# Kernel optimization log

Measured on AMD Instinct MI355X. Metric: run time of the kernel, lower is better.

Reference implementation:

```python
import jax, jax.numpy as jnp
import numpy as np

D_MODEL = 1024
N_HEAD = 16
N_KV_HEAD = 4
HEAD_DIM = D_MODEL // N_HEAD  # 64
N_GROUP = N_HEAD // N_KV_HEAD  # 4
ROPE_BASE = 10000.0
ROPE_DIM = HEAD_DIM  # rope_percentage = 1.0


def _rope_tables(seq_len, dtype):
    half = ROPE_DIM // 2
    inv_freq = 1.0 / (ROPE_BASE ** (jnp.arange(0, half, dtype=jnp.float32) * 2.0 / ROPE_DIM))
    pos = jnp.arange(seq_len, dtype=jnp.float32)
    freqs = pos[:, None] * inv_freq[None, :]  # [S, half]
    return jnp.cos(freqs).astype(dtype), jnp.sin(freqs).astype(dtype)


def _apply_rope(t):
    # t: [B, H, S, D]; rotate first ROPE_DIM dims (split-half convention)
    S = t.shape[2]
    cos, sin = _rope_tables(S, t.dtype)  # [S, half]
    half = ROPE_DIM // 2
    t1 = t[..., :half]
    t2 = t[..., half:ROPE_DIM]
    rot = jnp.concatenate([t1 * cos - t2 * sin, t1 * sin + t2 * cos], axis=-1)
    if ROPE_DIM < t.shape[-1]:
        rot = jnp.concatenate([rot, t[..., ROPE_DIM:]], axis=-1)
    return rot


def setup_inputs() -> dict:
    key = jax.random.key(0)
    ks = jax.random.split(key, 5)
    B, S = 1, 4096
    sd = 1.0 / np.sqrt(D_MODEL)
    x = jax.random.normal(ks[0], (B, S, D_MODEL), dtype=jnp.float32)
    w_q = jax.random.normal(ks[1], (D_MODEL, N_HEAD * HEAD_DIM), dtype=jnp.float32) * sd
    w_k = jax.random.normal(ks[2], (D_MODEL, N_KV_HEAD * HEAD_DIM), dtype=jnp.float32) * sd
    w_v = jax.random.normal(ks[3], (D_MODEL, N_KV_HEAD * HEAD_DIM), dtype=jnp.float32) * sd
    w_o = jax.random.normal(ks[4], (D_MODEL, D_MODEL), dtype=jnp.float32) * sd
    return {"x": x, "w_q": w_q, "w_k": w_k, "w_v": w_v, "w_o": w_o}


def reference(x, w_q, w_k, w_v, w_o):
    B, S, _ = x.shape
    q = (x @ w_q).reshape(B, S, N_HEAD, HEAD_DIM).transpose(0, 2, 1, 3)     # [B,H,S,D]
    k = (x @ w_k).reshape(B, S, N_KV_HEAD, HEAD_DIM).transpose(0, 2, 1, 3)  # [B,Hk,S,D]
    v = (x @ w_v).reshape(B, S, N_KV_HEAD, HEAD_DIM).transpose(0, 2, 1, 3)
    q = _apply_rope(q)
    k = _apply_rope(k)
    # repeat KV heads to match query heads (ops.repeat along head axis)
    k = jnp.repeat(k, N_GROUP, axis=1)  # [B,H,S,D]
    v = jnp.repeat(v, N_GROUP, axis=1)
    scale = 1.0 / jnp.sqrt(jnp.asarray(HEAD_DIM, dtype=x.dtype))
    scores = jnp.einsum("bhqd,bhkd->bhqk", q, k) * scale
    attn = jax.nn.softmax(scores, axis=-1)
    out = jnp.einsum("bhqk,bhkd->bhqd", attn, v)  # [B,H,S,D]
    out = out.transpose(0, 2, 1, 3).reshape(B, S, D_MODEL)
    return out @ w_o
```

## Files before the change

### kernel.cpp

```cpp
#include <hip/hip_runtime.h>
#include <math.h>

#define S_LEN 4096
#define DMODEL 1024
#define NHEAD 16
#define NKV 4
#define HDIM 64
#define QSCALE 0.125f

typedef __attribute__((ext_vector_type(8))) short bf16x8;
typedef __attribute__((ext_vector_type(4))) float f32x4;

static __device__ __forceinline__ unsigned short f2bf(float f) {
  unsigned int u = __float_as_uint(f);
  u += 0x7fffu + ((u >> 16) & 1u);
  return (unsigned short)(u >> 16);
}

static __device__ __forceinline__ void gload_lds16(const unsigned short* g, unsigned short* l) {
  __builtin_amdgcn_global_load_lds((const __attribute__((address_space(1))) void*)g,
                                   (__attribute__((address_space(3))) void*)l, 16, 0, 0);
}

__global__ void k_cast4(const float* __restrict__ in, unsigned short* __restrict__ out) {
  int i = blockIdx.x * blockDim.x + threadIdx.x;
  if (i >= S_LEN * DMODEL / 4) return;
  f32x4 v = *(const f32x4*)(in + (size_t)i * 4);
  union { unsigned short us[4]; uint2 d; } o;
#pragma unroll
  for (int j = 0; j < 4; ++j) o.us[j] = f2bf(v[j]);
  *(uint2*)(out + (size_t)i * 4) = o.d;
}

__global__ __launch_bounds__(256) void k_prepw(const float* __restrict__ wq, const float* __restrict__ wk,
                                               const float* __restrict__ wv, const float* __restrict__ wo,
                                               unsigned short* __restrict__ wqkvT, unsigned short* __restrict__ woT) {
  __shared__ float T[64][65];
  int b = blockIdx.x;
  const float* src;
  unsigned short* dst;
  int srcN, n0, k0, scol;
  if (b < 384) {
    int rt = b >> 4, kt = b & 15;
    n0 = rt * 64; k0 = kt * 64;
    if (n0 < 1024) { src = wq; srcN = 1024; scol = n0; }
    else if (n0 < 1280) { src = wk; srcN = 256; scol = n0 - 1024; }
    else { src = wv; srcN = 256; scol = n0 - 1280; }
    dst = wqkvT;
  } else {
    int bb = b - 384;
    int rt = bb >> 4, kt = bb & 15;
    n0 = rt * 64; k0 = kt * 64;
    src = wo; srcN = 1024; scol = n0; dst = woT;
  }
  int tr = threadIdx.x >> 6, tc = threadIdx.x & 63;
#pragma unroll
  for (int i = 0; i < 16; ++i) {
    int kk = i * 4 + tr;
    T[kk][tc] = src[(size_t)(k0 + kk) * srcN + scol + tc];
  }
  __syncthreads();
#pragma unroll
  for (int i = 0; i < 16; ++i) {
    int nn = i * 4 + tr;
    dst[(size_t)(n0 + nn) * 1024 + k0 + tc] = f2bf(T[tc][nn]);
  }
}

__global__ void k_rope_tables(float* __restrict__ ct, float* __restrict__ st) {
  int i = blockIdx.x * blockDim.x + threadIdx.x;
  if (i >= S_LEN * 32) return;
  int s = i >> 5, d = i & 31;
  float inv = expf(-(float)d * (1.0f / 32.0f) * logf(10000.0f));
  float f = (float)s * inv;
  ct[i] = cosf(f);
  st[i] = sinf(f);
}

__global__ __launch_bounds__(256) void k_gemmQKV(const unsigned short* __restrict__ A,
                                                 const unsigned short* __restrict__ BT,
                                                 const float* __restrict__ ct, const float* __restrict__ st,
                                                 unsigned short* __restrict__ Qb, unsigned short* __restrict__ Kh,
                                                 unsigned short* __restrict__ Vb) {
  __shared__ unsigned short As[128 * 64];
  __shared__ unsigned short Bs[128 * 64];
  const int tid = threadIdx.x;
  const int lane = tid & 63, wid = tid >> 6;
  const int r = lane & 15, g = lane >> 4;
  const int wm = wid >> 1, wn = wid & 1;
  const int bn0 = blockIdx.x << 7;
  const int bm0 = blockIdx.y << 7;

  f32x4 acc[4][4];
#pragma unroll
  for (int mt = 0; mt < 4; ++mt)
#pragma unroll
    for (int nt = 0; nt < 4; ++nt) acc[mt][nt] = 0.0f;

  for (int k0 = 0; k0 < 1024; k0 += 64) {
#pragma unroll
    for (int i = 0; i < 4; ++i) {
      int c = i * 256 + tid;
      int row = c >> 3, slot = c & 7;
      int ss = slot ^ (row & 7);
      int lbase = (i * 256 + (tid & ~63)) * 8;
      gload_lds16(A + (size_t)(bm0 + row) * 1024 + k0 + ss * 8, &As[lbase]);
      gload_lds16(BT + (size_t)(bn0 + row) * 1024 + k0 + ss * 8, &Bs[lbase]);
    }
    __syncthreads();
#pragma unroll
    for (int h = 0; h < 2; ++h) {
      bf16x8 am[4], bn[4];
#pragma unroll
      for (int mt = 0; mt < 4; ++mt) {
        int row = wm * 64 + mt * 16 + r;
        int slot = (g + 4 * h) ^ (row & 7);
        am[mt] = *(const bf16x8*)&As[row * 64 + slot * 8];
      }
#pragma unroll
      for (int nt = 0; nt < 4; ++nt) {
        int row = wn * 64 + nt * 16 + r;
        int slot = (g + 4 * h) ^ (row & 7);
        bn[nt] = *(const bf16x8*)&Bs[row * 64 + slot * 8];
      }
#pragma unroll
      for (int mt = 0; mt < 4; ++mt)
#pragma unroll
        for (int nt = 0; nt < 4; ++nt)
          acc[mt][nt] = __builtin_amdgcn_mfma_f32_16x16x32_bf16(am[mt], bn[nt], acc[mt][nt], 0, 0, 0);
    }
    __syncthreads();
  }

  const int colbase = bn0 + wn * 64;
  const int srow0 = bm0 + wm * 64;
  if (colbase < 1024) {
#pragma unroll
    for (int mt = 0; mt < 4; ++mt)
#pragma unroll
      for (int q = 0; q < 4; ++q) {
        int srow = srow0 + mt * 16 + g * 4 + q;
#pragma unroll
        for (int ntp = 0; ntp < 2; ++ntp) {
          int di = ntp * 16 + r;
          float t1 = acc[mt][ntp][q], t2 = acc[mt][ntp + 2][q];
          float c = ct[srow * 32 + di], s = st[srow * 32 + di];
          Qb[(size_t)srow * 1024 + colbase + di] = f2bf((t1 * c - t2 * s) * QSCALE);
          Qb[(size_t)srow * 1024 + colbase + di + 32] = f2bf((t1 * s + t2 * c) * QSCALE);
        }
      }
  } else if (colbase < 1280) {
    const int kvh = (colbase - 1024) >> 6;
#pragma unroll
    for (int mt = 0; mt < 4; ++mt)
#pragma unroll
      for (int q = 0; q < 4; ++q) {
        int srow = srow0 + mt * 16 + g * 4 + q;
#pragma unroll
        for (int ntp = 0; ntp < 2; ++ntp) {
          int di = ntp * 16 + r;
          float t1 = acc[mt][ntp][q], t2 = acc[mt][ntp + 2][q];
          float c = ct[srow * 32 + di], s = st[srow * 32 + di];
          Kh[((size_t)kvh * S_LEN + srow) * 64 + di] = f2bf(t1 * c - t2 * s);
          Kh[((size_t)kvh * S_LEN + srow) * 64 + di + 32] = f2bf(t1 * s + t2 * c);
        }
      }
  } else {
    const int vcol = colbase - 1280;
#pragma unroll
    for (int mt = 0; mt < 4; ++mt)
#pragma unroll
      for (int nt = 0; nt < 4; ++nt)
#pragma unroll
        for (int q = 0; q < 4; ++q)
          Vb[(size_t)(srow0 + mt * 16 + g * 4 + q) * 256 + vcol + nt * 16 + r] = f2bf(acc[mt][nt][q]);
  }
}

__global__ void k_vperm(const unsigned short* __restrict__ Vb, unsigned short* __restrict__ VP) {
  int i4 = blockIdx.x * blockDim.x + threadIdx.x;
  if (i4 >= NKV * HDIM * S_LEN / 4) return;
  int i = i4 * 4;
  int s = i & (S_LEN - 1);
  int d = (i >> 12) & 63;
  int kvh = i >> 18;
  int base = s & ~63;
  int p64 = s & 63;
  int u = p64 >> 5, g = (p64 >> 3) & 3, jq = (p64 >> 2) & 1;
  int koff0 = 32 * u + 16 * jq + 4 * g;
  const unsigned short* src = Vb + (size_t)(base + koff0) * 256 + kvh * 64 + d;
  union { unsigned short us[4]; uint2 dd; } o;
#pragma unroll
  for (int j = 0; j < 4; ++j) o.us[j] = src[(size_t)j * 256];
  *(uint2*)(VP + i) = o.dd;
}

__global__ __launch_bounds__(256) void k_gemm128(const unsigned short* __restrict__ A,
                                                 const unsigned short* __restrict__ BT,
                                                 float* __restrict__ C, int M, int N, int K) {
  __shared__ unsigned short As[128 * 64];
  __shared__ unsigned short Bs[128 * 64];
  const int tid = threadIdx.x;
  const int lane = tid & 63, wid = tid >> 6;
  const int r = lane & 15, g = lane >> 4;
  const int wm = wid >> 1, wn = wid & 1;
  const int bn0 = blockIdx.x << 7;
  const int bm0 = blockIdx.y << 7;

  f32x4 acc[4][4];
#pragma unroll
  for (int mt = 0; mt < 4; ++mt)
#pragma unroll
    for (int nt = 0; nt < 4; ++nt) acc[mt][nt] = 0.0f;

  for (int k0 = 0; k0 < K; k0 += 64) {
#pragma unroll
    for (int i = 0; i < 4; ++i) {
      int c = i * 256 + tid;
      int row = c >> 3, slot = c & 7;
      int ss = slot ^ (row & 7);
      int lbase = (i * 256 + (tid & ~63)) * 8;
      gload_lds16(A + (size_t)(bm0 + row) * K + k0 + ss * 8, &As[lbase]);
      gload_lds16(BT + (size_t)(bn0 + row) * K + k0 + ss * 8, &Bs[lbase]);
    }
    __syncthreads();
#pragma unroll
    for (int h = 0; h < 2; ++h) {
      bf16x8 am[4], bn[4];
#pragma unroll
      for (int mt = 0; mt < 4; ++mt) {
        int row = wm * 64 + mt * 16 + r;
        int slot = (g + 4 * h) ^ (row & 7);
        am[mt] = *(const bf16x8*)&As[row * 64 + slot * 8];
      }
#pragma unroll
      for (int nt = 0; nt < 4; ++nt) {
        int row = wn * 64 + nt * 16 + r;
        int slot = (g + 4 * h) ^ (row & 7);
        bn[nt] = *(const bf16x8*)&Bs[row * 64 + slot * 8];
      }
#pragma unroll
      for (int mt = 0; mt < 4; ++mt)
#pragma unroll
        for (int nt = 0; nt < 4; ++nt)
          acc[mt][nt] = __builtin_amdgcn_mfma_f32_16x16x32_bf16(am[mt], bn[nt], acc[mt][nt], 0, 0, 0);
    }
    __syncthreads();
  }
#pragma unroll
  for (int mt = 0; mt < 4; ++mt)
#pragma unroll
    for (int nt = 0; nt < 4; ++nt)
#pragma unroll
      for (int q = 0; q < 4; ++q)
        C[(size_t)(bm0 + wm * 64 + mt * 16 + g * 4 + q) * N + bn0 + wn * 64 + nt * 16 + r] = acc[mt][nt][q];
}

__global__ __launch_bounds__(256, 2) void k_attn(const unsigned short* __restrict__ Q,
                                                 const unsigned short* __restrict__ Kh,
                                                 const unsigned short* __restrict__ VP,
                                                 unsigned short* __restrict__ Ab) {
  __shared__ unsigned short sm[2][2][4096];
  const int tid = threadIdx.x;
  const int wave = tid >> 6, lane = tid & 63;
  const int r = lane & 15, g = lane >> 4;
  const int kvh = blockIdx.y;
  const int head = kvh * 4 + wave;
  const int qbase = blockIdx.x * 32;
  const int bidx = (lane & 48) >> 2;

  const unsigned short* khb = Kh + (size_t)kvh * S_LEN * 64;
  const unsigned short* vpb = VP + (size_t)kvh * S_LEN * 64;

  bf16x8 qf[2][2];
#pragma unroll
  for (int c = 0; c < 2; ++c)
#pragma unroll
    for (int h0 = 0; h0 < 2; ++h0)
      qf[c][h0] = *(const bf16x8*)(Q + (size_t)(qbase + 16 * c + r) * DMODEL + head * HDIM + 32 * h0 + 8 * g);

  f32x4 Oa[2][4];
#pragma unroll
  for (int c = 0; c < 2; ++c)
#pragma unroll
    for (int dt = 0; dt < 4; ++dt) Oa[c][dt] = 0.0f;
  float m_[2] = {-INFINITY, -INFINITY};
  float l_[2] = {0.0f, 0.0f};

  auto stage = [&](int b, int kv0) {
#pragma unroll
    for (int i = 0; i < 2; ++i) {
      int row = i * 32 + (tid >> 3), slot = tid & 7;
      int cs = slot ^ (row & 7);
      int lbase = (i * 256 + (tid & ~63)) * 8;
      gload_lds16(khb + (size_t)(kv0 + row) * 64 + cs * 8, &sm[b][0][lbase]);
      gload_lds16(vpb + (size_t)row * S_LEN + kv0 + cs * 8, &sm[b][1][lbase]);
    }
  };

  stage(0, 0);
  asm volatile("s_waitcnt vmcnt(0)" ::: "memory");
  __syncthreads();

  for (int t = 0; t < 64; ++t) {
    const int buf = t & 1;
    if (t < 63) stage(buf ^ 1, (t + 1) * 64);

    bf16x8 kf[4][2], vf[4][2];
#pragma unroll
    for (int tt = 0; tt < 4; ++tt) {
      int row = 16 * tt + r;
#pragma unroll
      for (int h = 0; h < 2; ++h) {
        int slot = (g + 4 * h) ^ (r & 7);
        kf[tt][h] = *(const bf16x8*)&sm[buf][0][row * 64 + slot * 8];
        vf[tt][h] = *(const bf16x8*)&sm[buf][1][row * 64 + slot * 8];
      }
    }
    f32x4 sc[2][4];
#pragma unroll
    for (int tt = 0; tt < 4; ++tt)
#pragma unroll
      for (int c = 0; c < 2; ++c) {
        f32x4 a = 0.0f;
        a = __builtin_amdgcn_mfma_f32_16x16x32_bf16(kf[tt][0], qf[c][0], a, 0, 0, 0);
        a = __builtin_amdgcn_mfma_f32_16x16x32_bf16(kf[tt][1], qf[c][1], a, 0, 0, 0);
        sc[c][tt] = a;
      }
    bf16x8 pa[2][2];
    bool resc[2];
    float bsc[2][4];
#pragma unroll
    for (int c = 0; c < 2; ++c) {
      float a0 = fmaxf(fmaxf(sc[c][0][0], sc[c][0][1]), fmaxf(sc[c][0][2], sc[c][0][3]));
      float a1 = fmaxf(fmaxf(sc[c][1][0], sc[c][1][1]), fmaxf(sc[c][1][2], sc[c][1][3]));
      float a2 = fmaxf(fmaxf(sc[c][2][0], sc[c][2][1]), fmaxf(sc[c][2][2], sc[c][2][3]));
      float a3 = fmaxf(fmaxf(sc[c][3][0], sc[c][3][1]), fmaxf(sc[c][3][2], sc[c][3][3]));
      float tm = fmaxf(fmaxf(a0, a1), fmaxf(a2, a3));
      tm = fmaxf(tm, __shfl_xor(tm, 16, 64));
      tm = fmaxf(tm, __shfl_xor(tm, 32, 64));
      bool defer = __all(tm <= m_[c] + 8.0f);
      float mn = m_[c];
      float scl = 1.0f;
      if (!defer) {
        mn = fmaxf(m_[c], tm);
        scl = __expf(m_[c] - mn);
        m_[c] = mn;
      }
      resc[c] = !defer;
      float s0 = 0.f, s1 = 0.f, s2 = 0.f, s3 = 0.f;
#pragma unroll
      for (int p = 0; p < 4; ++p) {
        sc[c][0][p] = __expf(sc[c][0][p] - mn); s0 += sc[c][0][p];
        sc[c][1][p] = __expf(sc[c][1][p] - mn); s1 += sc[c][1][p];
        sc[c][2][p] = __expf(sc[c][2][p] - mn); s2 += sc[c][2][p];
        sc[c][3][p] = __expf(sc[c][3][p] - mn); s3 += sc[c][3][p];
      }
      float ts = (s0 + s1) + (s2 + s3);
      ts += __shfl_xor(ts, 16, 64);
      ts += __shfl_xor(ts, 32, 64);
      l_[c] = l_[c] * scl + ts;
      if (!defer) {
#pragma unroll
        for (int p = 0; p < 4; ++p) bsc[c][p] = __shfl(scl, bidx + p, 64);
      }
#pragma unroll
      for (int u = 0; u < 2; ++u) {
        union { bf16x8 v; unsigned short us[8]; } pk;
#pragma unroll
        for (int j = 0; j < 4; ++j) {
          pk.us[j] = f2bf(sc[c][2 * u][j]);
          pk.us[4 + j] = f2bf(sc[c][2 * u + 1][j]);
        }
        pa[c][u] = pk.v;
      }
    }
#pragma unroll
    for (int c = 0; c < 2; ++c)
      if (resc[c]) {
#pragma unroll
        for (int dt = 0; dt < 4; ++dt)
#pragma unroll
          for (int p = 0; p < 4; ++p) Oa[c][dt][p] *= bsc[c][p];
      }
#pragma unroll
    for (int dt = 0; dt < 4; ++dt)
#pragma unroll
      for (int c = 0; c < 2; ++c) {
        Oa[c][dt] = __builtin_amdgcn_mfma_f32_16x16x32_bf16(pa[c][0], vf[dt][0], Oa[c][dt], 0, 0, 0);
        Oa[c][dt] = __builtin_amdgcn_mfma_f32_16x16x32_bf16(pa[c][1], vf[dt][1], Oa[c][dt], 0, 0, 0);
      }
    asm volatile("s_waitcnt vmcnt(0)" ::: "memory");
    __syncthreads();
  }
#pragma unroll
  for (int c = 0; c < 2; ++c) {
    float li = 1.0f / l_[c];
    float bl[4];
#pragma unroll
    for (int p = 0; p < 4; ++p) bl[p] = __shfl(li, bidx + p, 64);
#pragma unroll
    for (int dt = 0; dt < 4; ++dt)
#pragma unroll
      for (int p = 0; p < 4; ++p)
        Ab[(size_t)(qbase + 16 * c + 4 * g + p) * DMODEL + head * HDIM + 16 * dt + r] =
            f2bf(Oa[c][dt][p] * bl[p]);
  }
}

extern "C" void kernel_launch(void* const* d_in, const int* in_sizes, int n_in,
                              void* d_out, int out_size, void* d_ws, size_t ws_size,
                              hipStream_t stream) {
  const float* x   = (const float*)d_in[0];
  const float* w_q = (const float*)d_in[1];
  const float* w_k = (const float*)d_in[2];
  const float* w_v = (const float*)d_in[3];
  const float* w_o = (const float*)d_in[4];
  float* out = (float*)d_out;

  char* ws = (char*)d_ws;
  size_t off = 0;
  auto alloc = [&](size_t bytes) -> void* {
    void* p = ws + off;
    off = (off + bytes + 255) & ~(size_t)255;
    return p;
  };
  unsigned short* xb    = (unsigned short*)alloc((size_t)S_LEN * DMODEL * 2);
  unsigned short* wqkvT = (unsigned short*)alloc((size_t)1536 * DMODEL * 2);
  unsigned short* woT   = (unsigned short*)alloc((size_t)DMODEL * DMODEL * 2);
  float* ct = (float*)alloc((size_t)S_LEN * 32 * 4);
  float* st = (float*)alloc((size_t)S_LEN * 32 * 4);
  unsigned short* Qb = (unsigned short*)alloc((size_t)S_LEN * DMODEL * 2);
  unsigned short* Kh = (unsigned short*)alloc((size_t)NKV * S_LEN * HDIM * 2);
  unsigned short* Vb = (unsigned short*)alloc((size_t)S_LEN * 256 * 2);
  unsigned short* VP = (unsigned short*)alloc((size_t)NKV * HDIM * S_LEN * 2);
  unsigned short* Ab = (unsigned short*)alloc((size_t)S_LEN * DMODEL * 2);

  k_cast4<<<(S_LEN * DMODEL / 4 + 255) / 256, 256, 0, stream>>>(x, xb);
  k_prepw<<<640, 256, 0, stream>>>(w_q, w_k, w_v, w_o, wqkvT, woT);
  k_rope_tables<<<(S_LEN * 32 + 255) / 256, 256, 0, stream>>>(ct, st);

  k_gemmQKV<<<dim3(1536 / 128, S_LEN / 128), 256, 0, stream>>>(xb, wqkvT, ct, st, Qb, Kh, Vb);
  k_vperm<<<(NKV * HDIM * S_LEN / 4 + 255) / 256, 256, 0, stream>>>(Vb, VP);

  k_attn<<<dim3(S_LEN / 32, NKV), 256, 0, stream>>>(Qb, Kh, VP, Ab);

  k_gemm128<<<dim3(DMODEL / 128, S_LEN / 128), 256, 0, stream>>>(Ab, woT, out, S_LEN, DMODEL, DMODEL);
}
```

Before: 256.4 us.

## Halve attention query tile per block and use exp2 with deferred row reductions

```diff
diff --git a/kernel.cpp b/kernel.cpp
--- a/kernel.cpp
+++ b/kernel.cpp
@@ -1,4 +1,5 @@
 #include <hip/hip_runtime.h>
+#include <hip/hip_bf16.h>
 #include <math.h>
 
 #define S_LEN 4096
@@ -6,7 +7,7 @@
 #define NHEAD 16
 #define NKV 4
 #define HDIM 64
-#define QSCALE 0.125f
+#define QSCALE 0.18033688011112042f
 
 typedef __attribute__((ext_vector_type(8))) short bf16x8;
 typedef __attribute__((ext_vector_type(4))) float f32x4;
@@ -15,6 +16,16 @@
   unsigned int u = __float_as_uint(f);
   u += 0x7fffu + ((u >> 16) & 1u);
   return (unsigned short)(u >> 16);
+}
+
+static __device__ __forceinline__ unsigned short f2bf_hw(float f) {
+  union { __hip_bfloat16 h; unsigned short u; } cv;
+  cv.h = __float2bfloat16(f);
+  return cv.u;
+}
+
+static __device__ __forceinline__ float fexp2(float x) {
+  return __builtin_amdgcn_exp2f(x);
 }
 
 static __device__ __forceinline__ void gload_lds16(const unsigned short* g, unsigned short* l) {
@@ -256,7 +267,7 @@
         C[(size_t)(bm0 + wm * 64 + mt * 16 + g * 4 + q) * N + bn0 + wn * 64 + nt * 16 + r] = acc[mt][nt][q];
 }
 
-__global__ __launch_bounds__(256, 2) void k_attn(const unsigned short* __restrict__ Q,
+__global__ __launch_bounds__(256, 4) void k_attn(const unsigned short* __restrict__ Q,
                                                  const unsigned short* __restrict__ Kh,
                                                  const unsigned short* __restrict__ VP,
                                                  unsigned short* __restrict__ Ab) {
@@ -264,28 +275,25 @@
   const int tid = threadIdx.x;
   const int wave = tid >> 6, lane = tid & 63;
   const int r = lane & 15, g = lane >> 4;
-  const int kvh = blockIdx.y;
+  const int bid = blockIdx.x;
+  const int kvh = bid & 3;
+  const int qbase = (((bid >> 3) << 1) + ((bid >> 2) & 1)) * 16;
   const int head = kvh * 4 + wave;
-  const int qbase = blockIdx.x * 32;
   const int bidx = (lane & 48) >> 2;
 
   const unsigned short* khb = Kh + (size_t)kvh * S_LEN * 64;
   const unsigned short* vpb = VP + (size_t)kvh * S_LEN * 64;
 
-  bf16x8 qf[2][2];
-#pragma unroll
-  for (int c = 0; c < 2; ++c)
-#pragma unroll
-    for (int h0 = 0; h0 < 2; ++h0)
-      qf[c][h0] = *(const bf16x8*)(Q + (size_t)(qbase + 16 * c + r) * DMODEL + head * HDIM + 32 * h0 + 8 * g);
-
-  f32x4 Oa[2][4];
-#pragma unroll
-  for (int c = 0; c < 2; ++c)
-#pragma unroll
-    for (int dt = 0; dt < 4; ++dt) Oa[c][dt] = 0.0f;
-  float m_[2] = {-INFINITY, -INFINITY};
-  float l_[2] = {0.0f, 0.0f};
+  bf16x8 qf[2];
+#pragma unroll
+  for (int h0 = 0; h0 < 2; ++h0)
+    qf[h0] = *(const bf16x8*)(Q + (size_t)(qbase + r) * DMODEL + head * HDIM + 32 * h0 + 8 * g);
+
+  f32x4 Oa[4];
+#pragma unroll
+  for (int dt = 0; dt < 4; ++dt) Oa[dt] = 0.0f;
+  float m_ = -INFINITY;
+  float l_ = 0.0f;
 
   auto stage = [&](int b, int kv0) {
 #pragma unroll
@@ -317,95 +325,79 @@
         vf[tt][h] = *(const bf16x8*)&sm[buf][1][row * 64 + slot * 8];
       }
     }
-    f32x4 sc[2][4];
-#pragma unroll
-    for (int tt = 0; tt < 4; ++tt)
-#pragma unroll
-      for (int c = 0; c < 2; ++c) {
-        f32x4 a = 0.0f;
-        a = __builtin_amdgcn_mfma_f32_16x16x32_bf16(kf[tt][0], qf[c][0], a, 0, 0, 0);
-        a = __builtin_amdgcn_mfma_f32_16x16x32_bf16(kf[tt][1], qf[c][1], a, 0, 0, 0);
-        sc[c][tt] = a;
-      }
-    bf16x8 pa[2][2];
-    bool resc[2];
-    float bsc[2][4];
-#pragma unroll
-    for (int c = 0; c < 2; ++c) {
-      float a0 = fmaxf(fmaxf(sc[c][0][0], sc[c][0][1]), fmaxf(sc[c][0][2], sc[c][0][3]));
-      float a1 = fmaxf(fmaxf(sc[c][1][0], sc[c][1][1]), fmaxf(sc[c][1][2], sc[c][1][3]));
-      float a2 = fmaxf(fmaxf(sc[c][2][0], sc[c][2][1]), fmaxf(sc[c][2][2], sc[c][2][3]));
-      float a3 = fmaxf(fmaxf(sc[c][3][0], sc[c][3][1]), fmaxf(sc[c][3][2], sc[c][3][3]));
-      float tm = fmaxf(fmaxf(a0, a1), fmaxf(a2, a3));
+    f32x4 sc[4];
+#pragma unroll
+    for (int tt = 0; tt < 4; ++tt) {
+      f32x4 a = 0.0f;
+      a = __builtin_amdgcn_mfma_f32_16x16x32_bf16(kf[tt][0], qf[0], a, 0, 0, 0);
+      a = __builtin_amdgcn_mfma_f32_16x16x32_bf16(kf[tt][1], qf[1], a, 0, 0, 0);
+      sc[tt] = a;
+    }
+    float a0 = fmaxf(fmaxf(sc[0][0], sc[0][1]), fmaxf(sc[0][2], sc[0][3]));
+    float a1 = fmaxf(fmaxf(sc[1][0], sc[1][1]), fmaxf(sc[1][2], sc[1][3]));
+    float a2 = fmaxf(fmaxf(sc[2][0], sc[2][1]), fmaxf(sc[2][2], sc[2][3]));
+    float a3 = fmaxf(fmaxf(sc[3][0], sc[3][1]), fmaxf(sc[3][2], sc[3][3]));
+    float tm = fmaxf(fmaxf(a0, a1), fmaxf(a2, a3));
+    bool defer = __all(tm <= m_ + 8.0f);
+    float mn = m_;
+    float scl = 1.0f;
+    if (!defer) {
       tm = fmaxf(tm, __shfl_xor(tm, 16, 64));
       tm = fmaxf(tm, __shfl_xor(tm, 32, 64));
-      bool defer = __all(tm <= m_[c] + 8.0f);
-      float mn = m_[c];
-      float scl = 1.0f;
-      if (!defer) {
-        mn = fmaxf(m_[c], tm);
-        scl = __expf(m_[c] - mn);
-        m_[c] = mn;
-      }
-      resc[c] = !defer;
-      float s0 = 0.f, s1 = 0.f, s2 = 0.f, s3 = 0.f;
-#pragma unroll
-      for (int p = 0; p < 4; ++p) {
-        sc[c][0][p] = __expf(sc[c][0][p] - mn); s0 += sc[c][0][p];
-        sc[c][1][p] = __expf(sc[c][1][p] - mn); s1 += sc[c][1][p];
-        sc[c][2][p] = __expf(sc[c][2][p] - mn); s2 += sc[c][2][p];
-        sc[c][3][p] = __expf(sc[c][3][p] - mn); s3 += sc[c][3][p];
-      }
-      float ts = (s0 + s1) + (s2 + s3);
-      ts += __shfl_xor(ts, 16, 64);
-      ts += __shfl_xor(ts, 32, 64);
-      l_[c] = l_[c] * scl + ts;
-      if (!defer) {
-#pragma unroll
-        for (int p = 0; p < 4; ++p) bsc[c][p] = __shfl(scl, bidx + p, 64);
-      }
-#pragma unroll
-      for (int u = 0; u < 2; ++u) {
-        union { bf16x8 v; unsigned short us[8]; } pk;
-#pragma unroll
-        for (int j = 0; j < 4; ++j) {
-          pk.us[j] = f2bf(sc[c][2 * u][j]);
-          pk.us[4 + j] = f2bf(sc[c][2 * u + 1][j]);
-        }
-        pa[c][u] = pk.v;
-      }
-    }
-#pragma unroll
-    for (int c = 0; c < 2; ++c)
-      if (resc[c]) {
-#pragma unroll
-        for (int dt = 0; dt < 4; ++dt)
-#pragma unroll
-          for (int p = 0; p < 4; ++p) Oa[c][dt][p] *= bsc[c][p];
-      }
-#pragma unroll
-    for (int dt = 0; dt < 4; ++dt)
-#pragma unroll
-      for (int c = 0; c < 2; ++c) {
-        Oa[c][dt] = __builtin_amdgcn_mfma_f32_16x16x32_bf16(pa[c][0], vf[dt][0], Oa[c][dt], 0, 0, 0);
-        Oa[c][dt] = __builtin_amdgcn_mfma_f32_16x16x32_bf16(pa[c][1], vf[dt][1], Oa[c][dt], 0, 0, 0);
-      }
+      mn = fmaxf(m_, tm);
+      scl = fexp2(m_ - mn);
+      m_ = mn;
+    }
+    float s0 = 0.f, s1 = 0.f, s2 = 0.f, s3 = 0.f;
+#pragma unroll
+    for (int p = 0; p < 4; ++p) {
+      sc[0][p] = fexp2(sc[0][p] - mn); s0 += sc[0][p];
+      sc[1][p] = fexp2(sc[1][p] - mn); s1 += sc[1][p];
+      sc[2][p] = fexp2(sc[2][p] - mn); s2 += sc[2][p];
+      sc[3][p] = fexp2(sc[3][p] - mn); s3 += sc[3][p];
+    }
+    l_ = l_ * scl + ((s0 + s1) + (s2 + s3));
+    bf16x8 pa[2];
+#pragma unroll
+    for (int u = 0; u < 2; ++u) {
+      union { bf16x8 v; unsigned short us[8]; } pk;
+#pragma unroll
+      for (int j = 0; j < 4; ++j) {
+        pk.us[j] = f2bf_hw(sc[2 * u][j]);
+        pk.us[4 + j] = f2bf_hw(sc[2 * u + 1][j]);
+      }
+      pa[u] = pk.v;
+    }
+    if (!defer) {
+      float bsc[4];
+#pragma unroll
+      for (int p = 0; p < 4; ++p) bsc[p] = __shfl(scl, bidx + p, 64);
+#pragma unroll
+      for (int dt = 0; dt < 4; ++dt)
+#pragma unroll
+        for (int p = 0; p < 4; ++p) Oa[dt][p] *= bsc[p];
+    }
+#pragma unroll
+    for (int dt = 0; dt < 4; ++dt) {
+      Oa[dt] = __builtin_amdgcn_mfma_f32_16x16x32_bf16(pa[0], vf[dt][0], Oa[dt], 0, 0, 0);
+      Oa[dt] = __builtin_amdgcn_mfma_f32_16x16x32_bf16(pa[1], vf[dt][1], Oa[dt], 0, 0, 0);
+    }
     asm volatile("s_waitcnt vmcnt(0)" ::: "memory");
     __syncthreads();
   }
-#pragma unroll
-  for (int c = 0; c < 2; ++c) {
-    float li = 1.0f / l_[c];
-    float bl[4];
-#pragma unroll
-    for (int p = 0; p < 4; ++p) bl[p] = __shfl(li, bidx + p, 64);
-#pragma unroll
-    for (int dt = 0; dt < 4; ++dt)
-#pragma unroll
-      for (int p = 0; p < 4; ++p)
-        Ab[(size_t)(qbase + 16 * c + 4 * g + p) * DMODEL + head * HDIM + 16 * dt + r] =
-            f2bf(Oa[c][dt][p] * bl[p]);
-  }
+  float lt = l_;
+  lt += __shfl_xor(lt, 16, 64);
+  lt += __shfl_xor(lt, 32, 64);
+  float li = 1.0f / lt;
+  float bl[4];
+#pragma unroll
+  for (int p = 0; p < 4; ++p) bl[p] = __shfl(li, bidx + p, 64);
+#pragma unroll
+  for (int dt = 0; dt < 4; ++dt)
+#pragma unroll
+    for (int p = 0; p < 4; ++p)
+      Ab[(size_t)(qbase + 4 * g + p) * DMODEL + head * HDIM + 16 * dt + r] =
+          f2bf(Oa[dt][p] * bl[p]);
 }
 
 extern "C" void kernel_launch(void* const* d_in, const int* in_sizes, int n_in,
@@ -443,7 +435,7 @@
   k_gemmQKV<<<dim3(1536 / 128, S_LEN / 128), 256, 0, stream>>>(xb, wqkvT, ct, st, Qb, Kh, Vb);
   k_vperm<<<(NKV * HDIM * S_LEN / 4 + 255) / 256, 256, 0, stream>>>(Vb, VP);
 
-  k_attn<<<dim3(S_LEN / 32, NKV), 256, 0, stream>>>(Qb, Kh, VP, Ab);
+  k_attn<<<1024, 256, 0, stream>>>(Qb, Kh, VP, Ab);
 
   k_gemm128<<<dim3(DMODEL / 128, S_LEN / 128), 256, 0, stream>>>(Ab, woT, out, S_LEN, DMODEL, DMODEL);
 }
```

Measured after the change: 230.6 us. -10.1%, faster.
